# Performance work log

Hardware: AMD Instinct MI355X
Metric: run time of the kernel (lower is better)

The kernel has to match this reference:

```python
import jax, jax.numpy as jnp
import numpy as np

N_Q = 8          # number of residual quantizer stages
N_CODES = 1024   # 2 ** (75 // N_q + 1)
D = 128
GAMMA = 0.99


def setup_inputs() -> dict:
    key = jax.random.key(0)
    k1, k2, k3, k4 = jax.random.split(key, 4)
    data_object = jax.random.normal(k1, (16, D, 2048), dtype=jnp.float32)
    weights = jax.random.normal(k2, (N_Q, N_CODES, D), dtype=jnp.float32)
    # EMA cluster-size buffer; scale so most codes are 'alive' (>= 2)
    N_i = jax.random.uniform(k3, (N_Q, N_CODES), dtype=jnp.float32) * 100.0
    m_i = jax.random.normal(k4, (N_Q, N_CODES, D), dtype=jnp.float32)
    return {"data_object": data_object, "weights": weights, "N_i": N_i, "m_i": m_i}


def reference(data_object, weights, N_i, m_i):
    b, d, s = data_object.shape
    y = jnp.transpose(data_object, (0, 2, 1))  # [b, s, D]
    residual = y
    cur_y = jnp.zeros_like(y)
    all_idx, new_Ni, new_mi, new_W = [], [], [], []
    key = jax.random.key(42)
    one_m_g = 1.0 - GAMMA
    for i in range(N_Q):
        W = weights[i]  # [N, D]
        # squared euclidean distances: ||y||^2 + ||W||^2 - 2 y.W^T  -> [b, s, N]
        dist = ((residual ** 2).sum(-1)[..., None]
                + (W ** 2).sum(-1)[None, None, :]
                - 2.0 * jnp.einsum('bsd,nd->bsn', residual, W))
        idx = jnp.argmin(dist, axis=-1)          # [b, s]
        Q = W[idx]                               # gather  [b, s, D]
        cur_y = cur_y + Q
        flat_idx = idx.reshape(-1)               # [b*s]
        flat_res = residual.reshape(-1, d)       # [b*s, D]
        # fused scatter-reduce replacing the torch per-code mask loop
        counts = jax.ops.segment_sum(jnp.ones(flat_idx.shape, jnp.float32),
                                     flat_idx, num_segments=N_CODES)
        sums = jax.ops.segment_sum(flat_res, flat_idx, num_segments=N_CODES)
        Ni_new = N_i[i] * GAMMA + counts * one_m_g
        mi_new = m_i[i] * GAMMA + sums * one_m_g
        w_new = mi_new / jnp.clip(Ni_new, 1e-8)[:, None]
        # dead-code replacement with random residual vectors
        dead = Ni_new < 2.0
        rid = jax.random.randint(jax.random.fold_in(key, i), (N_CODES,),
                                 0, flat_res.shape[0])
        w_new = jnp.where(dead[:, None], flat_res[rid], w_new)
        all_idx.append(idx)
        new_Ni.append(Ni_new)
        new_mi.append(mi_new)
        new_W.append(w_new)
        residual = residual - Q
    cur_y_t = jnp.transpose(cur_y, (0, 2, 1))  # [b, D, s]
    # straight-through estimator
    logits = data_object + jax.lax.stop_gradient(cur_y_t - data_object)
    commitment_loss = jnp.mean((jax.lax.stop_gradient(cur_y_t) - data_object) ** 2)
    indices = jnp.stack(all_idx, axis=0)  # [N_q, b, s]
    return (logits, commitment_loss, indices,
            jnp.stack(new_Ni), jnp.stack(new_mi), jnp.stack(new_W))
```

## Files before the change

### kernel.cpp

```cpp
#include <hip/hip_runtime.h>
#include <hip/hip_bf16.h>

#define NQ 8
#define NC 1024
#define DD 128
#define BB 16
#define SS 2048
#define RR (BB * SS)
#define GAMMA_F 0.99f
#define TAU 0.03f

typedef __attribute__((ext_vector_type(8))) short bf16x8;
typedef __attribute__((ext_vector_type(4))) float f32x4;

__device__ __forceinline__ ushort f2bf(float x) {
  __hip_bfloat16 b = __float2bfloat16(x);
  return *reinterpret_cast<ushort*>(&b);
}
__device__ __forceinline__ float bf2f(ushort u) {
  unsigned v = ((unsigned)u) << 16;
  return *reinterpret_cast<float*>(&v);
}

__global__ __launch_bounds__(256) void k_transpose_in(
    const float* __restrict__ data, float* __restrict__ res)
{
  __shared__ float tile[32][33];
  int b = blockIdx.z;
  int s0 = blockIdx.x << 5, d0 = blockIdx.y << 5;
  int tx = threadIdx.x, ty = threadIdx.y;
  #pragma unroll
  for (int r = 0; r < 32; r += 8)
    tile[ty + r][tx] = data[((size_t)b * DD + d0 + ty + r) * SS + s0 + tx];
  __syncthreads();
  #pragma unroll
  for (int r = 0; r < 32; r += 8)
    res[((size_t)b * SS + s0 + ty + r) * DD + d0 + tx] = tile[tx][ty + r];
}

__global__ void k_wsq(const float* __restrict__ W, float* __restrict__ wsq)
{
  int c = blockIdx.x * blockDim.x + threadIdx.x;
  if (c >= NQ * NC) return;
  const float4* p = reinterpret_cast<const float4*>(W + (size_t)c * DD);
  float s = 0.f;
  #pragma unroll 8
  for (int k = 0; k < DD / 4; ++k) {
    float4 v = p[k];
    s += v.x * v.x + v.y * v.y + v.z * v.z + v.w * v.w;
  }
  wsq[c] = s;
}

__global__ __launch_bounds__(256) void k_split(
    const float* __restrict__ src, ushort* __restrict__ dst)
{
  int i = blockIdx.x * 256 + threadIdx.x;
  int row = i >> 2, ks = i & 3;
  const float4* sp = reinterpret_cast<const float4*>(src + (size_t)row * DD + ks * 32);
  size_t gb = ((size_t)(row >> 4) * 8 + ks * 2) * 64 + (row & 15);
  #pragma unroll
  for (int kg = 0; kg < 4; ++kg) {
    float4 a = sp[kg * 2], b = sp[kg * 2 + 1];
    ushort4 h0, h1, l0, l1;
    h0.x = f2bf(a.x); l0.x = f2bf(a.x - bf2f(h0.x));
    h0.y = f2bf(a.y); l0.y = f2bf(a.y - bf2f(h0.y));
    h0.z = f2bf(a.z); l0.z = f2bf(a.z - bf2f(h0.z));
    h0.w = f2bf(a.w); l0.w = f2bf(a.w - bf2f(h0.w));
    h1.x = f2bf(b.x); l1.x = f2bf(b.x - bf2f(h1.x));
    h1.y = f2bf(b.y); l1.y = f2bf(b.y - bf2f(h1.y));
    h1.z = f2bf(b.z); l1.z = f2bf(b.z - bf2f(h1.z));
    h1.w = f2bf(b.w); l1.w = f2bf(b.w - bf2f(h1.w));
    ushort* ph = dst + (gb + kg * 16) * 8;
    *reinterpret_cast<ushort4*>(ph) = h0;
    *reinterpret_cast<ushort4*>(ph + 4) = h1;
    ushort* pl = ph + 64 * 8;
    *reinterpret_cast<ushort4*>(pl) = l0;
    *reinterpret_cast<ushort4*>(pl + 4) = l1;
  }
}

__global__ __launch_bounds__(256, 3) void k_argmin(
    const ushort* __restrict__ res_hl, const ushort* __restrict__ w_hl,
    const float* __restrict__ wsq,
    int* __restrict__ idxw, float* __restrict__ idxf,
    int* __restrict__ count, int* __restrict__ fb_count,
    int* __restrict__ fb_list, int stage)
{
  const int t = threadIdx.x;
  const int l = t & 63;
  const int w = t >> 6;
  const int l15 = l & 15;
  const int row0 = blockIdx.x * 64;
  const float* wsqs = wsq + stage * NC;
  const ushort* wb = w_hl + (size_t)stage * NC * 256;

  const size_t ab = ((size_t)(row0 >> 4) + w) * 8;
  bf16x8 ah[4], al[4];
  #pragma unroll
  for (int ks = 0; ks < 4; ++ks) {
    ah[ks] = *reinterpret_cast<const bf16x8*>(res_hl + ((ab + ks * 2) * 64 + l) * 8);
    al[ks] = *reinterpret_cast<const bf16x8*>(res_hl + ((ab + ks * 2 + 1) * 64 + l) * 8);
  }

  float m1[4], m2[4];
  int i1[4];
  #pragma unroll
  for (int rg = 0; rg < 4; ++rg) { m1[rg] = 3.4e38f; m2[rg] = 3.4e38f; i1[rg] = 0; }

  bf16x8 bh0[4], bl0[4], bh1[4], bl1[4];

#define LOADB(BH, BL, CT) {                                                       \
    size_t bb = (size_t)(CT) * 8;                                                 \
    _Pragma("unroll")                                                             \
    for (int ks = 0; ks < 4; ++ks) {                                              \
      BH[ks] = *reinterpret_cast<const bf16x8*>(wb + ((bb + ks * 2) * 64 + l) * 8);        \
      BL[ks] = *reinterpret_cast<const bf16x8*>(wb + ((bb + ks * 2 + 1) * 64 + l) * 8);    \
    } }

#define COMPUTE(BH, BL, CT) {                                                     \
    f32x4 accP = {0.f, 0.f, 0.f, 0.f};                                            \
    f32x4 accQ = {0.f, 0.f, 0.f, 0.f};                                            \
    _Pragma("unroll")                                                             \
    for (int ks = 0; ks < 4; ++ks) {                                              \
      accP = __builtin_amdgcn_mfma_f32_16x16x32_bf16(ah[ks], BH[ks], accP, 0, 0, 0); \
      accQ = __builtin_amdgcn_mfma_f32_16x16x32_bf16(al[ks], BH[ks], accQ, 0, 0, 0); \
      accQ = __builtin_amdgcn_mfma_f32_16x16x32_bf16(ah[ks], BL[ks], accQ, 0, 0, 0); \
    }                                                                             \
    int code = (CT) * 16 + l15;                                                   \
    float sq = wsqs[code];                                                        \
    _Pragma("unroll")                                                             \
    for (int rg = 0; rg < 4; ++rg) {                                              \
      float s = fmaf(-2.f, accP[rg] + accQ[rg], sq);                              \
      if (s < m1[rg]) { m2[rg] = m1[rg]; m1[rg] = s; i1[rg] = code; }             \
      else if (s < m2[rg]) m2[rg] = s;                                            \
    } }

  LOADB(bh0, bl0, 0);
  for (int ct = 0; ct < 64; ct += 2) {
    LOADB(bh1, bl1, ct + 1);
    COMPUTE(bh0, bl0, ct);
    if (ct + 2 < 64) LOADB(bh0, bl0, ct + 2);
    COMPUTE(bh1, bl1, ct + 1);
  }
#undef LOADB
#undef COMPUTE

  #pragma unroll
  for (int mk = 1; mk <= 8; mk <<= 1) {
    #pragma unroll
    for (int rg = 0; rg < 4; ++rg) {
      float om1 = __shfl_xor(m1[rg], mk);
      int   oi  = __shfl_xor(i1[rg], mk);
      float om2 = __shfl_xor(m2[rg], mk);
      bool bwin = (om1 < m1[rg]) || (om1 == m1[rg] && oi < i1[rg]);
      float lose = bwin ? m1[rg] : om1;
      m2[rg] = fminf(fminf(m2[rg], om2), lose);
      if (bwin) { m1[rg] = om1; i1[rg] = oi; }
    }
  }
  if (l15 == 0) {
    int kg = l >> 4;
    #pragma unroll
    for (int rg = 0; rg < 4; ++rg) {
      int row = row0 + w * 16 + kg * 4 + rg;
      if (m2[rg] - m1[rg] > TAU) {
        idxw[row] = i1[rg];
        idxf[row] = (float)i1[rg];
        atomicAdd(&count[i1[rg]], 1);
      } else {
        int p = atomicAdd(fb_count, 1);
        fb_list[p] = row;
      }
    }
  }
}

__global__ __launch_bounds__(256) void k_fallback(
    const float* __restrict__ res, const float* __restrict__ W,
    const float* __restrict__ wsq, const int* __restrict__ fb_count,
    const int* __restrict__ fb_list,
    int* __restrict__ idxw, float* __restrict__ idxf,
    int* __restrict__ count, int stage)
{
  __shared__ float rr[128];
  __shared__ float sv[256];
  __shared__ int   si[256];
  int n = *fb_count;
  int t = threadIdx.x;
  for (int b = blockIdx.x; b < n; b += gridDim.x) {
    int row = fb_list[b];
    __syncthreads();
    if (t < 128) rr[t] = res[(size_t)row * DD + t];
    __syncthreads();
    float bm = 3.4e38f; int bi = 0;
    #pragma unroll
    for (int j = 0; j < 4; ++j) {
      int c = t + j * 256;
      const float4* wp = reinterpret_cast<const float4*>(W + ((size_t)stage * NC + c) * DD);
      float dot = 0.f;
      #pragma unroll 8
      for (int k = 0; k < 32; ++k) {
        float4 wv = wp[k];
        dot = fmaf(rr[4 * k + 0], wv.x, dot);
        dot = fmaf(rr[4 * k + 1], wv.y, dot);
        dot = fmaf(rr[4 * k + 2], wv.z, dot);
        dot = fmaf(rr[4 * k + 3], wv.w, dot);
      }
      float s = fmaf(-2.f, dot, wsq[stage * NC + c]);
      if (s < bm || (s == bm && c < bi)) { bm = s; bi = c; }
    }
    sv[t] = bm; si[t] = bi;
    __syncthreads();
    for (int sft = 128; sft > 0; sft >>= 1) {
      if (t < sft) {
        float ov = sv[t + sft]; int oi = si[t + sft];
        if (ov < sv[t] || (ov == sv[t] && oi < si[t])) { sv[t] = ov; si[t] = oi; }
      }
      __syncthreads();
    }
    if (t == 0) {
      int win = si[0];
      idxw[row] = win;
      idxf[row] = (float)win;
      atomicAdd(&count[win], 1);
    }
  }
}

__global__ __launch_bounds__(1024) void k_scan(
    int* __restrict__ count, int* __restrict__ offs, int* __restrict__ pos)
{
  __shared__ int sc[1024];
  int t = threadIdx.x;
  sc[t] = count[t];
  __syncthreads();
  for (int off = 1; off < 1024; off <<= 1) {
    int v = (t >= off) ? sc[t - off] : 0;
    __syncthreads();
    sc[t] += v;
    __syncthreads();
  }
  offs[t + 1] = sc[t];
  if (t == 0) { offs[0] = 0; count[1024] = 0; }
  pos[t] = 0;
  count[t] = 0;
}

__global__ __launch_bounds__(256) void k_scatter(
    const int* __restrict__ idxw, const int* __restrict__ offs,
    int* __restrict__ pos, int* __restrict__ rows_sorted)
{
  int r = blockIdx.x * 256 + threadIdx.x;
  int c = idxw[r];
  int slot = offs[c] + atomicAdd(&pos[c], 1);
  rows_sorted[slot] = r;
}

__device__ __forceinline__ unsigned rotl32(unsigned v, int r) { return (v << r) | (v >> (32 - r)); }

__device__ void threefry2x32(unsigned ks0, unsigned ks1, unsigned x0, unsigned x1,
                             unsigned& o0, unsigned& o1)
{
  unsigned ks2 = ks0 ^ ks1 ^ 0x1BD11BDAu;
  x0 += ks0; x1 += ks1;
  x0 += x1; x1 = rotl32(x1, 13); x1 ^= x0;
  x0 += x1; x1 = rotl32(x1, 15); x1 ^= x0;
  x0 += x1; x1 = rotl32(x1, 26); x1 ^= x0;
  x0 += x1; x1 = rotl32(x1, 6);  x1 ^= x0;
  x0 += ks1; x1 += ks2 + 1u;
  x0 += x1; x1 = rotl32(x1, 17); x1 ^= x0;
  x0 += x1; x1 = rotl32(x1, 29); x1 ^= x0;
  x0 += x1; x1 = rotl32(x1, 16); x1 ^= x0;
  x0 += x1; x1 = rotl32(x1, 24); x1 ^= x0;
  x0 += ks2; x1 += ks0 + 2u;
  x0 += x1; x1 = rotl32(x1, 13); x1 ^= x0;
  x0 += x1; x1 = rotl32(x1, 15); x1 ^= x0;
  x0 += x1; x1 = rotl32(x1, 26); x1 ^= x0;
  x0 += x1; x1 = rotl32(x1, 6);  x1 ^= x0;
  x0 += ks0; x1 += ks1 + 3u;
  x0 += x1; x1 = rotl32(x1, 17); x1 ^= x0;
  x0 += x1; x1 = rotl32(x1, 29); x1 ^= x0;
  x0 += x1; x1 = rotl32(x1, 16); x1 ^= x0;
  x0 += x1; x1 = rotl32(x1, 24); x1 ^= x0;
  x0 += ks1; x1 += ks2 + 4u;
  x0 += x1; x1 = rotl32(x1, 13); x1 ^= x0;
  x0 += x1; x1 = rotl32(x1, 15); x1 ^= x0;
  x0 += x1; x1 = rotl32(x1, 26); x1 ^= x0;
  x0 += x1; x1 = rotl32(x1, 6);  x1 ^= x0;
  x0 += ks2; x1 += ks0 + 5u;
  o0 = x0; o1 = x1;
}

__global__ __launch_bounds__(1024) void k_finalize(
    const float* __restrict__ Ni_in, const float* __restrict__ mi_in,
    const int* __restrict__ offs, const int* __restrict__ rows_sorted,
    const float* __restrict__ res_cur,
    float* __restrict__ outNi, float* __restrict__ outmi, float* __restrict__ outW,
    int stage)
{
  __shared__ float red[8][128];
  const float ONEMG = (float)(1.0 - 0.99);
  int c = blockIdx.x;
  int t = threadIdx.x;
  int d = t & 127;
  int jw = t >> 7;
  int base = offs[c];
  int cnt = offs[c + 1] - base;
  const int* rs = rows_sorted + base;

  float sum = 0.f;
  int j = jw;
  for (; j + 24 < cnt; j += 32) {
    int r0 = rs[j];
    int r1 = rs[j + 8];
    int r2 = rs[j + 16];
    int r3 = rs[j + 24];
    float v0 = res_cur[(size_t)r0 * DD + d];
    float v1 = res_cur[(size_t)r1 * DD + d];
    float v2 = res_cur[(size_t)r2 * DD + d];
    float v3 = res_cur[(size_t)r3 * DD + d];
    sum += v0 + v1 + v2 + v3;
  }
  for (; j < cnt; j += 8)
    sum += res_cur[(size_t)rs[j] * DD + d];

  red[jw][d] = sum;
  __syncthreads();

  if (jw == 0) {
    float s = red[0][d] + red[1][d] + red[2][d] + red[3][d]
            + red[4][d] + red[5][d] + red[6][d] + red[7][d];
    float ni = Ni_in[stage * NC + c] * GAMMA_F + (float)cnt * ONEMG;
    float mm = mi_in[((size_t)stage * NC + c) * DD + d] * GAMMA_F + s * ONEMG;
    float w = mm / fmaxf(ni, 1e-8f);
    if (ni < 2.0f) {
      unsigned K0, K1, a0, a1, b0, b1, o0, o1;
      threefry2x32(0u, 42u, 0u, (unsigned)stage, K0, K1);
      threefry2x32(K0, K1, 0u, 2u, a0, a1);
      threefry2x32(K0, K1, 1u, 3u, b0, b1);
      unsigned bits;
      if (c < 512) { threefry2x32(a1, b1, (unsigned)c, (unsigned)(c + 512), o0, o1); bits = o0; }
      else         { threefry2x32(a1, b1, (unsigned)(c - 512), (unsigned)c, o0, o1); bits = o1; }
      int rid = (int)(bits & 32767u);
      w = res_cur[(size_t)rid * DD + d];
    }
    if (d == 0) outNi[stage * NC + c] = ni;
    size_t o = ((size_t)stage * NC + c) * DD + d;
    outmi[o] = mm;
    outW[o] = w;
  }
}

__global__ __launch_bounds__(256) void k_update(
    float* __restrict__ res, const float* __restrict__ W,
    const int* __restrict__ idx, ushort* __restrict__ res_hl, int stage)
{
  int row = blockIdx.x * 16 + (threadIdx.x >> 4);
  int g = threadIdx.x & 15;
  int id = idx[row];
  const float4* rp = reinterpret_cast<const float4*>(res + (size_t)row * DD + g * 8);
  const float4* qp = reinterpret_cast<const float4*>(W + ((size_t)stage * NC + id) * DD + g * 8);
  float4 r0 = rp[0], r1 = rp[1];
  float4 q0 = qp[0], q1 = qp[1];
  float4 o0, o1;
  o0.x = r0.x - q0.x; o0.y = r0.y - q0.y; o0.z = r0.z - q0.z; o0.w = r0.w - q0.w;
  o1.x = r1.x - q1.x; o1.y = r1.y - q1.y; o1.z = r1.z - q1.z; o1.w = r1.w - q1.w;
  float4* wp2 = reinterpret_cast<float4*>(res + (size_t)row * DD + g * 8);
  wp2[0] = o0; wp2[1] = o1;
  ushort4 h0, h1, l0, l1;
  h0.x = f2bf(o0.x); l0.x = f2bf(o0.x - bf2f(h0.x));
  h0.y = f2bf(o0.y); l0.y = f2bf(o0.y - bf2f(h0.y));
  h0.z = f2bf(o0.z); l0.z = f2bf(o0.z - bf2f(h0.z));
  h0.w = f2bf(o0.w); l0.w = f2bf(o0.w - bf2f(h0.w));
  h1.x = f2bf(o1.x); l1.x = f2bf(o1.x - bf2f(h1.x));
  h1.y = f2bf(o1.y); l1.y = f2bf(o1.y - bf2f(h1.y));
  h1.z = f2bf(o1.z); l1.z = f2bf(o1.z - bf2f(h1.z));
  h1.w = f2bf(o1.w); l1.w = f2bf(o1.w - bf2f(h1.w));
  int ks = g >> 2, kg = g & 3;
  size_t gb = ((size_t)(row >> 4) * 8 + ks * 2) * 64 + kg * 16 + (row & 15);
  ushort* ph = res_hl + gb * 8;
  *reinterpret_cast<ushort4*>(ph) = h0;
  *reinterpret_cast<ushort4*>(ph + 4) = h1;
  ushort* pl = ph + 64 * 8;
  *reinterpret_cast<ushort4*>(pl) = l0;
  *reinterpret_cast<ushort4*>(pl + 4) = l1;
}

__global__ __launch_bounds__(256) void k_final(
    const float* __restrict__ data, const float* __restrict__ res,
    float* __restrict__ logits, float* __restrict__ partials)
{
  __shared__ float tile[32][33];
  __shared__ float wsum[4];
  int b = blockIdx.z, s0 = blockIdx.x << 5, d0 = blockIdx.y << 5;
  int tx = threadIdx.x, ty = threadIdx.y;
  #pragma unroll
  for (int r = 0; r < 32; r += 8)
    tile[ty + r][tx] = res[((size_t)b * SS + s0 + ty + r) * DD + d0 + tx];
  __syncthreads();
  float l = 0.f;
  #pragma unroll
  for (int r = 0; r < 32; r += 8) {
    int dv = d0 + ty + r, s = s0 + tx;
    size_t o = ((size_t)b * DD + dv) * SS + s;
    float rv = tile[tx][ty + r];
    logits[o] = data[o] - rv;
    l = fmaf(rv, rv, l);
  }
  #pragma unroll
  for (int m = 1; m < 64; m <<= 1) l += __shfl_xor(l, m);
  int lin = ty * 32 + tx;
  if ((lin & 63) == 0) wsum[lin >> 6] = l;
  __syncthreads();
  if (lin == 0) {
    int bl = (blockIdx.z * gridDim.y + blockIdx.y) * gridDim.x + blockIdx.x;
    partials[bl] = wsum[0] + wsum[1] + wsum[2] + wsum[3];
  }
}

__global__ __launch_bounds__(1024) void k_loss_reduce(
    const float* __restrict__ partials, float* __restrict__ loss)
{
  __shared__ float ws[16];
  int t = threadIdx.x;
  float s = partials[t] + partials[t + 1024] + partials[t + 2048] + partials[t + 3072];
  #pragma unroll
  for (int m = 1; m < 64; m <<= 1) s += __shfl_xor(s, m);
  if ((t & 63) == 0) ws[t >> 6] = s;
  __syncthreads();
  if (t < 16) {
    float v = ws[t];
    #pragma unroll
    for (int m = 1; m < 16; m <<= 1) v += __shfl_xor(v, m);
    if (t == 0) loss[0] = v * (1.0f / 4194304.0f);
  }
}

extern "C" void kernel_launch(void* const* d_in, const int* in_sizes, int n_in,
                              void* d_out, int out_size, void* d_ws, size_t ws_size,
                              hipStream_t stream)
{
  (void)in_sizes; (void)n_in; (void)out_size; (void)ws_size;
  const float* data = (const float*)d_in[0];
  const float* W    = (const float*)d_in[1];
  const float* Ni   = (const float*)d_in[2];
  const float* mi   = (const float*)d_in[3];

  float* out        = (float*)d_out;
  float* out_logits = out;
  float* out_loss   = out + (size_t)BB * DD * SS;
  float* out_idx    = out_loss + 1;
  float* out_Ni     = out_idx + (size_t)NQ * RR;
  float* out_mi     = out_Ni + (size_t)NQ * NC;
  float* out_W      = out_mi + (size_t)NQ * NC * DD;

  char* wp = (char*)d_ws;
  float*  resA        = (float*)wp;   wp += (size_t)RR * DD * 4;
  ushort* res_hl      = (ushort*)wp;  wp += (size_t)RR * DD * 4;
  ushort* w_hl        = (ushort*)wp;  wp += (size_t)NQ * NC * DD * 4;
  float*  wsq         = (float*)wp;   wp += (size_t)NQ * NC * 4;
  int*    idxw        = (int*)wp;     wp += (size_t)RR * 4;
  int*    fb_list     = (int*)wp;     wp += (size_t)RR * 4;
  int*    rows_sorted = (int*)wp;     wp += (size_t)RR * 4;
  int*    count       = (int*)wp;     wp += (size_t)1025 * 4;
  int*    fb_count    = count + 1024;
  int*    pos         = (int*)wp;     wp += (size_t)NC * 4;
  int*    offs        = (int*)wp;     wp += (size_t)(NC + 1) * 4;
  float*  partials    = (float*)wp;   wp += (size_t)4096 * 4;

  k_transpose_in<<<dim3(SS / 32, DD / 32, BB), dim3(32, 8), 0, stream>>>(data, resA);
  k_split<<<RR * 4 / 256, 256, 0, stream>>>(resA, res_hl);
  k_wsq<<<(NQ * NC + 255) / 256, 256, 0, stream>>>(W, wsq);
  k_split<<<NQ * NC * 4 / 256, 256, 0, stream>>>(W, w_hl);
  hipMemsetAsync(count, 0, 1025 * sizeof(int), stream);

  for (int i = 0; i < NQ; ++i) {
    k_argmin<<<RR / 64, 256, 0, stream>>>(res_hl, w_hl, wsq, idxw,
                                          out_idx + (size_t)i * RR,
                                          count, fb_count, fb_list, i);
    k_fallback<<<512, 256, 0, stream>>>(resA, W, wsq, fb_count, fb_list,
                                        idxw, out_idx + (size_t)i * RR, count, i);
    k_scan<<<1, 1024, 0, stream>>>(count, offs, pos);
    k_scatter<<<RR / 256, 256, 0, stream>>>(idxw, offs, pos, rows_sorted);
    k_finalize<<<NC, 1024, 0, stream>>>(Ni, mi, offs, rows_sorted, resA,
                                        out_Ni, out_mi, out_W, i);
    k_update<<<RR / 16, 256, 0, stream>>>(resA, W, idxw, res_hl, i);
  }

  k_final<<<dim3(SS / 32, DD / 32, BB), dim3(32, 8), 0, stream>>>(data, resA, out_logits, partials);
  k_loss_reduce<<<1, 1024, 0, stream>>>(partials, out_loss);
}
```

Baseline: 965.3 us.

## Fuse residual update into argmin and split codebook search across warps

The argmin kernel now handles 16 rows per block, with each of the four warps scanning a quarter of the codebook. Partial minima are merged through shared memory, and the same kernel subtracts the chosen code and rewrites the fp32 and bf16 hi/lo residuals. The fallback kernel does the same update for ambiguous rows, so the separate update kernel is removed. Finalize then rebuilds the pre-update residual sums as post-update residual plus count times the codeword, which adds a small rounding difference; the four-times-larger grid re-reads the codebook more often from cache.

```diff
diff --git a/kernel.cpp b/kernel.cpp
--- a/kernel.cpp
+++ b/kernel.cpp
@@ -80,22 +80,28 @@
   }
 }
 
-__global__ __launch_bounds__(256, 3) void k_argmin(
-    const ushort* __restrict__ res_hl, const ushort* __restrict__ w_hl,
+__global__ __launch_bounds__(256, 4) void k_argmin(
+    float* __restrict__ res, ushort* __restrict__ res_hl,
+    const ushort* __restrict__ w_hl, const float* __restrict__ W,
     const float* __restrict__ wsq,
     int* __restrict__ idxw, float* __restrict__ idxf,
     int* __restrict__ count, int* __restrict__ fb_count,
     int* __restrict__ fb_list, int stage)
 {
+  __shared__ float Lm1[4][16], Lm2[4][16];
+  __shared__ int   Li1[4][16];
+  __shared__ int   sidx[16];
+  __shared__ int   sfb[16];
+
   const int t = threadIdx.x;
   const int l = t & 63;
   const int w = t >> 6;
-  const int l15 = l & 15;
-  const int row0 = blockIdx.x * 64;
+  const int l15 = l & 15, kg = l >> 4;
+  const int row0 = blockIdx.x * 16;
   const float* wsqs = wsq + stage * NC;
   const ushort* wb = w_hl + (size_t)stage * NC * 256;
 
-  const size_t ab = ((size_t)(row0 >> 4) + w) * 8;
+  const size_t ab = (size_t)blockIdx.x * 8;
   bf16x8 ah[4], al[4];
   #pragma unroll
   for (int ks = 0; ks < 4; ++ks) {
@@ -108,43 +114,33 @@
   #pragma unroll
   for (int rg = 0; rg < 4; ++rg) { m1[rg] = 3.4e38f; m2[rg] = 3.4e38f; i1[rg] = 0; }
 
-  bf16x8 bh0[4], bl0[4], bh1[4], bl1[4];
-
-#define LOADB(BH, BL, CT) {                                                       \
-    size_t bb = (size_t)(CT) * 8;                                                 \
-    _Pragma("unroll")                                                             \
-    for (int ks = 0; ks < 4; ++ks) {                                              \
-      BH[ks] = *reinterpret_cast<const bf16x8*>(wb + ((bb + ks * 2) * 64 + l) * 8);        \
-      BL[ks] = *reinterpret_cast<const bf16x8*>(wb + ((bb + ks * 2 + 1) * 64 + l) * 8);    \
-    } }
-
-#define COMPUTE(BH, BL, CT) {                                                     \
-    f32x4 accP = {0.f, 0.f, 0.f, 0.f};                                            \
-    f32x4 accQ = {0.f, 0.f, 0.f, 0.f};                                            \
-    _Pragma("unroll")                                                             \
-    for (int ks = 0; ks < 4; ++ks) {                                              \
-      accP = __builtin_amdgcn_mfma_f32_16x16x32_bf16(ah[ks], BH[ks], accP, 0, 0, 0); \
-      accQ = __builtin_amdgcn_mfma_f32_16x16x32_bf16(al[ks], BH[ks], accQ, 0, 0, 0); \
-      accQ = __builtin_amdgcn_mfma_f32_16x16x32_bf16(ah[ks], BL[ks], accQ, 0, 0, 0); \
-    }                                                                             \
-    int code = (CT) * 16 + l15;                                                   \
-    float sq = wsqs[code];                                                        \
-    _Pragma("unroll")                                                             \
-    for (int rg = 0; rg < 4; ++rg) {                                              \
-      float s = fmaf(-2.f, accP[rg] + accQ[rg], sq);                              \
-      if (s < m1[rg]) { m2[rg] = m1[rg]; m1[rg] = s; i1[rg] = code; }             \
-      else if (s < m2[rg]) m2[rg] = s;                                            \
-    } }
-
-  LOADB(bh0, bl0, 0);
-  for (int ct = 0; ct < 64; ct += 2) {
-    LOADB(bh1, bl1, ct + 1);
-    COMPUTE(bh0, bl0, ct);
-    if (ct + 2 < 64) LOADB(bh0, bl0, ct + 2);
-    COMPUTE(bh1, bl1, ct + 1);
-  }
-#undef LOADB
-#undef COMPUTE
+  #pragma unroll 2
+  for (int k = 0; k < 16; ++k) {
+    int ct = w * 16 + k;
+    size_t bb = (size_t)ct * 8;
+    bf16x8 bh[4], bl[4];
+    #pragma unroll
+    for (int ks = 0; ks < 4; ++ks) {
+      bh[ks] = *reinterpret_cast<const bf16x8*>(wb + ((bb + ks * 2) * 64 + l) * 8);
+      bl[ks] = *reinterpret_cast<const bf16x8*>(wb + ((bb + ks * 2 + 1) * 64 + l) * 8);
+    }
+    f32x4 accP = {0.f, 0.f, 0.f, 0.f};
+    f32x4 accQ = {0.f, 0.f, 0.f, 0.f};
+    #pragma unroll
+    for (int ks = 0; ks < 4; ++ks) {
+      accP = __builtin_amdgcn_mfma_f32_16x16x32_bf16(ah[ks], bh[ks], accP, 0, 0, 0);
+      accQ = __builtin_amdgcn_mfma_f32_16x16x32_bf16(al[ks], bh[ks], accQ, 0, 0, 0);
+      accQ = __builtin_amdgcn_mfma_f32_16x16x32_bf16(ah[ks], bl[ks], accQ, 0, 0, 0);
+    }
+    int code = ct * 16 + l15;
+    float sq = wsqs[code];
+    #pragma unroll
+    for (int rg = 0; rg < 4; ++rg) {
+      float s = fmaf(-2.f, accP[rg] + accQ[rg], sq);
+      if (s < m1[rg]) { m2[rg] = m1[rg]; m1[rg] = s; i1[rg] = code; }
+      else if (s < m2[rg]) m2[rg] = s;
+    }
+  }
 
   #pragma unroll
   for (int mk = 1; mk <= 8; mk <<= 1) {
@@ -160,26 +156,80 @@
     }
   }
   if (l15 == 0) {
-    int kg = l >> 4;
     #pragma unroll
     for (int rg = 0; rg < 4; ++rg) {
-      int row = row0 + w * 16 + kg * 4 + rg;
-      if (m2[rg] - m1[rg] > TAU) {
-        idxw[row] = i1[rg];
-        idxf[row] = (float)i1[rg];
-        atomicAdd(&count[i1[rg]], 1);
-      } else {
-        int p = atomicAdd(fb_count, 1);
-        fb_list[p] = row;
-      }
+      Lm1[w][kg * 4 + rg] = m1[rg];
+      Lm2[w][kg * 4 + rg] = m2[rg];
+      Li1[w][kg * 4 + rg] = i1[rg];
+    }
+  }
+  __syncthreads();
+
+  if (t < 16) {
+    float gm1 = Lm1[0][t], gm2 = Lm2[0][t];
+    int gi = Li1[0][t];
+    #pragma unroll
+    for (int q = 1; q < 4; ++q) {
+      float b1 = Lm1[q][t], b2 = Lm2[q][t];
+      int bi = Li1[q][t];
+      bool bwin = (b1 < gm1) || (b1 == gm1 && bi < gi);
+      float lose = bwin ? gm1 : b1;
+      gm2 = fminf(fminf(gm2, b2), lose);
+      if (bwin) { gm1 = b1; gi = bi; }
+    }
+    int row = row0 + t;
+    if (gm2 - gm1 > TAU) {
+      idxw[row] = gi;
+      idxf[row] = (float)gi;
+      atomicAdd(&count[gi], 1);
+      sidx[t] = gi; sfb[t] = 0;
+    } else {
+      int p = atomicAdd(fb_count, 1);
+      fb_list[p] = row;
+      sidx[t] = 0; sfb[t] = 1;
+    }
+  }
+  __syncthreads();
+
+  {
+    int rloc = t >> 4, g = t & 15;
+    if (!sfb[rloc]) {
+      int row = row0 + rloc;
+      int id = sidx[rloc];
+      const float4* rp = reinterpret_cast<const float4*>(res + (size_t)row * DD + g * 8);
+      const float4* qp = reinterpret_cast<const float4*>(W + ((size_t)stage * NC + id) * DD + g * 8);
+      float4 r0 = rp[0], r1 = rp[1];
+      float4 q0 = qp[0], q1 = qp[1];
+      float4 o0, o1;
+      o0.x = r0.x - q0.x; o0.y = r0.y - q0.y; o0.z = r0.z - q0.z; o0.w = r0.w - q0.w;
+      o1.x = r1.x - q1.x; o1.y = r1.y - q1.y; o1.z = r1.z - q1.z; o1.w = r1.w - q1.w;
+      float4* wp2 = reinterpret_cast<float4*>(res + (size_t)row * DD + g * 8);
+      wp2[0] = o0; wp2[1] = o1;
+      ushort4 h0, h1, l0, l1;
+      h0.x = f2bf(o0.x); l0.x = f2bf(o0.x - bf2f(h0.x));
+      h0.y = f2bf(o0.y); l0.y = f2bf(o0.y - bf2f(h0.y));
+      h0.z = f2bf(o0.z); l0.z = f2bf(o0.z - bf2f(h0.z));
+      h0.w = f2bf(o0.w); l0.w = f2bf(o0.w - bf2f(h0.w));
+      h1.x = f2bf(o1.x); l1.x = f2bf(o1.x - bf2f(h1.x));
+      h1.y = f2bf(o1.y); l1.y = f2bf(o1.y - bf2f(h1.y));
+      h1.z = f2bf(o1.z); l1.z = f2bf(o1.z - bf2f(h1.z));
+      h1.w = f2bf(o1.w); l1.w = f2bf(o1.w - bf2f(h1.w));
+      int ks = g >> 2, kgg = g & 3;
+      size_t gb = ((size_t)(row >> 4) * 8 + ks * 2) * 64 + kgg * 16 + (row & 15);
+      ushort* ph = res_hl + gb * 8;
+      *reinterpret_cast<ushort4*>(ph) = h0;
+      *reinterpret_cast<ushort4*>(ph + 4) = h1;
+      ushort* pl = ph + 64 * 8;
+      *reinterpret_cast<ushort4*>(pl) = l0;
+      *reinterpret_cast<ushort4*>(pl + 4) = l1;
     }
   }
 }
 
 __global__ __launch_bounds__(256) void k_fallback(
-    const float* __restrict__ res, const float* __restrict__ W,
-    const float* __restrict__ wsq, const int* __restrict__ fb_count,
-    const int* __restrict__ fb_list,
+    float* __restrict__ res, ushort* __restrict__ res_hl,
+    const float* __restrict__ W, const float* __restrict__ wsq,
+    const int* __restrict__ fb_count, const int* __restrict__ fb_list,
     int* __restrict__ idxw, float* __restrict__ idxf,
     int* __restrict__ count, int stage)
 {
@@ -219,11 +269,20 @@
       }
       __syncthreads();
     }
+    int win = si[0];
     if (t == 0) {
-      int win = si[0];
       idxw[row] = win;
       idxf[row] = (float)win;
       atomicAdd(&count[win], 1);
+    }
+    if (t < 128) {
+      float o = rr[t] - W[((size_t)stage * NC + win) * DD + t];
+      res[(size_t)row * DD + t] = o;
+      ushort hi = f2bf(o);
+      ushort lo = f2bf(o - bf2f(hi));
+      size_t g0 = ((size_t)(row >> 4) * 8 + (t >> 5) * 2) * 64 + ((t >> 3) & 3) * 16 + (row & 15);
+      res_hl[g0 * 8 + (t & 7)] = hi;
+      res_hl[(g0 + 64) * 8 + (t & 7)] = lo;
     }
   }
 }
@@ -295,7 +354,8 @@
 __global__ __launch_bounds__(1024) void k_finalize(
     const float* __restrict__ Ni_in, const float* __restrict__ mi_in,
     const int* __restrict__ offs, const int* __restrict__ rows_sorted,
-    const float* __restrict__ res_cur,
+    const float* __restrict__ res, const float* __restrict__ W,
+    const int* __restrict__ idxw,
     float* __restrict__ outNi, float* __restrict__ outmi, float* __restrict__ outW,
     int stage)
 {
@@ -316,23 +376,25 @@
     int r1 = rs[j + 8];
     int r2 = rs[j + 16];
     int r3 = rs[j + 24];
-    float v0 = res_cur[(size_t)r0 * DD + d];
-    float v1 = res_cur[(size_t)r1 * DD + d];
-    float v2 = res_cur[(size_t)r2 * DD + d];
-    float v3 = res_cur[(size_t)r3 * DD + d];
+    float v0 = res[(size_t)r0 * DD + d];
+    float v1 = res[(size_t)r1 * DD + d];
+    float v2 = res[(size_t)r2 * DD + d];
+    float v3 = res[(size_t)r3 * DD + d];
     sum += v0 + v1 + v2 + v3;
   }
   for (; j < cnt; j += 8)
-    sum += res_cur[(size_t)rs[j] * DD + d];
+    sum += res[(size_t)rs[j] * DD + d];
 
   red[jw][d] = sum;
   __syncthreads();
 
   if (jw == 0) {
-    float s = red[0][d] + red[1][d] + red[2][d] + red[3][d]
-            + red[4][d] + red[5][d] + red[6][d] + red[7][d];
+    float s8 = red[0][d] + red[1][d] + red[2][d] + red[3][d]
+             + red[4][d] + red[5][d] + red[6][d] + red[7][d];
+    float wc = W[((size_t)stage * NC + c) * DD + d];
+    float sum_pre = fmaf((float)cnt, wc, s8);
     float ni = Ni_in[stage * NC + c] * GAMMA_F + (float)cnt * ONEMG;
-    float mm = mi_in[((size_t)stage * NC + c) * DD + d] * GAMMA_F + s * ONEMG;
+    float mm = mi_in[((size_t)stage * NC + c) * DD + d] * GAMMA_F + sum_pre * ONEMG;
     float w = mm / fmaxf(ni, 1e-8f);
     if (ni < 2.0f) {
       unsigned K0, K1, a0, a1, b0, b1, o0, o1;
@@ -343,48 +405,14 @@
       if (c < 512) { threefry2x32(a1, b1, (unsigned)c, (unsigned)(c + 512), o0, o1); bits = o0; }
       else         { threefry2x32(a1, b1, (unsigned)(c - 512), (unsigned)c, o0, o1); bits = o1; }
       int rid = (int)(bits & 32767u);
-      w = res_cur[(size_t)rid * DD + d];
+      int idr = idxw[rid];
+      w = res[(size_t)rid * DD + d] + W[((size_t)stage * NC + idr) * DD + d];
     }
     if (d == 0) outNi[stage * NC + c] = ni;
     size_t o = ((size_t)stage * NC + c) * DD + d;
     outmi[o] = mm;
     outW[o] = w;
   }
-}
-
-__global__ __launch_bounds__(256) void k_update(
-    float* __restrict__ res, const float* __restrict__ W,
-    const int* __restrict__ idx, ushort* __restrict__ res_hl, int stage)
-{
-  int row = blockIdx.x * 16 + (threadIdx.x >> 4);
-  int g = threadIdx.x & 15;
-  int id = idx[row];
-  const float4* rp = reinterpret_cast<const float4*>(res + (size_t)row * DD + g * 8);
-  const float4* qp = reinterpret_cast<const float4*>(W + ((size_t)stage * NC + id) * DD + g * 8);
-  float4 r0 = rp[0], r1 = rp[1];
-  float4 q0 = qp[0], q1 = qp[1];
-  float4 o0, o1;
-  o0.x = r0.x - q0.x; o0.y = r0.y - q0.y; o0.z = r0.z - q0.z; o0.w = r0.w - q0.w;
-  o1.x = r1.x - q1.x; o1.y = r1.y - q1.y; o1.z = r1.z - q1.z; o1.w = r1.w - q1.w;
-  float4* wp2 = reinterpret_cast<float4*>(res + (size_t)row * DD + g * 8);
-  wp2[0] = o0; wp2[1] = o1;
-  ushort4 h0, h1, l0, l1;
-  h0.x = f2bf(o0.x); l0.x = f2bf(o0.x - bf2f(h0.x));
-  h0.y = f2bf(o0.y); l0.y = f2bf(o0.y - bf2f(h0.y));
-  h0.z = f2bf(o0.z); l0.z = f2bf(o0.z - bf2f(h0.z));
-  h0.w = f2bf(o0.w); l0.w = f2bf(o0.w - bf2f(h0.w));
-  h1.x = f2bf(o1.x); l1.x = f2bf(o1.x - bf2f(h1.x));
-  h1.y = f2bf(o1.y); l1.y = f2bf(o1.y - bf2f(h1.y));
-  h1.z = f2bf(o1.z); l1.z = f2bf(o1.z - bf2f(h1.z));
-  h1.w = f2bf(o1.w); l1.w = f2bf(o1.w - bf2f(h1.w));
-  int ks = g >> 2, kg = g & 3;
-  size_t gb = ((size_t)(row >> 4) * 8 + ks * 2) * 64 + kg * 16 + (row & 15);
-  ushort* ph = res_hl + gb * 8;
-  *reinterpret_cast<ushort4*>(ph) = h0;
-  *reinterpret_cast<ushort4*>(ph + 4) = h1;
-  ushort* pl = ph + 64 * 8;
-  *reinterpret_cast<ushort4*>(pl) = l0;
-  *reinterpret_cast<ushort4*>(pl + 4) = l1;
 }
 
 __global__ __launch_bounds__(256) void k_final(
@@ -476,16 +504,15 @@
   hipMemsetAsync(count, 0, 1025 * sizeof(int), stream);
 
   for (int i = 0; i < NQ; ++i) {
-    k_argmin<<<RR / 64, 256, 0, stream>>>(res_hl, w_hl, wsq, idxw,
+    k_argmin<<<RR / 16, 256, 0, stream>>>(resA, res_hl, w_hl, W, wsq, idxw,
                                           out_idx + (size_t)i * RR,
                                           count, fb_count, fb_list, i);
-    k_fallback<<<512, 256, 0, stream>>>(resA, W, wsq, fb_count, fb_list,
+    k_fallback<<<512, 256, 0, stream>>>(resA, res_hl, W, wsq, fb_count, fb_list,
                                         idxw, out_idx + (size_t)i * RR, count, i);
     k_scan<<<1, 1024, 0, stream>>>(count, offs, pos);
     k_scatter<<<RR / 256, 256, 0, stream>>>(idxw, offs, pos, rows_sorted);
-    k_finalize<<<NC, 1024, 0, stream>>>(Ni, mi, offs, rows_sorted, resA,
+    k_finalize<<<NC, 1024, 0, stream>>>(Ni, mi, offs, rows_sorted, resA, W, idxw,
                                         out_Ni, out_mi, out_W, i);
-    k_update<<<RR / 16, 256, 0, stream>>>(resA, W, idxw, res_hl, i);
   }
 
   k_final<<<dim3(SS / 32, DD / 32, BB), dim3(32, 8), 0, stream>>>(data, resA, out_logits, partials);
```

Measured after the change: 836.9 us. -13.3%, faster.
